# Kernel optimization log

Measured on AMD Instinct MI355X. Metric: run time of the kernel, lower is better.

Reference implementation:

```python
import jax, jax.numpy as jnp
import numpy as np


def setup_inputs() -> dict:
    key = jax.random.key(0)
    k1, k2, k3, k4, k5 = jax.random.split(key, 5)
    N, L, H = 512, 512, 768
    num_texts = 32
    hidden_states = jax.random.normal(k1, (N, L, H), dtype=jnp.float32)
    attention_mask = jax.random.randint(k2, (N, L), 0, 2).astype(jnp.int32)
    sample_map = jnp.sort(jax.random.randint(k3, (N,), 0, num_texts).astype(jnp.int64))
    Wq = jax.random.normal(k4, (H, H), dtype=jnp.float32) * (1.0 / np.sqrt(H))
    bq = jnp.zeros((H,), dtype=jnp.float32)
    Wk = jax.random.normal(k5, (H, H), dtype=jnp.float32) * (1.0 / np.sqrt(H))
    bk = jnp.zeros((H,), dtype=jnp.float32)
    return {
        'hidden_states': hidden_states,
        'attention_mask': attention_mask,
        'sample_map': sample_map,
        'Wq': Wq, 'bq': bq, 'Wk': Wk, 'bk': bk,
        'num_texts': num_texts,
    }


def _attn_pool(hidden_states, mask, Wq, bq, Wk, bk):
    # hidden_states: [N, L, H]; mask: [N, L]
    H = hidden_states.shape[-1]
    # Q from mean over sequence (unmasked mean, as in original)
    q = jnp.einsum('nh,oh->no', hidden_states.mean(axis=1), Wq) + bq   # [N, H]
    k = jnp.einsum('nlh,oh->nlo', hidden_states, Wk) + bk              # [N, L, H]
    scores = jnp.einsum('nh,nlh->nl', q, k) / jnp.sqrt(jnp.float32(H))  # [N, L]
    scores = jnp.where(mask == 0, jnp.float32(-1e9), scores)
    alphas = jax.nn.softmax(scores, axis=1)                            # [N, L]
    return jnp.einsum('nl,nlh->nh', alphas, hidden_states)             # [N, H]


def reference(hidden_states, attention_mask, sample_map, Wq, bq, Wk, bk, num_texts):
    # dropout is identity in eval mode
    pooled = _attn_pool(hidden_states, attention_mask, Wq, bq, Wk, bk)  # [N, H]
    seg = sample_map.astype(jnp.int32)
    sums = jax.ops.segment_sum(pooled, seg, num_segments=num_texts)     # [T, H]
    counts = jax.ops.segment_sum(jnp.ones((pooled.shape[0],), pooled.dtype), seg,
                                 num_segments=num_texts)                # [T]
    counts = jnp.clip(counts, 1.0, None)
    return sums / counts[:, None]
```

## Files before the change

### kernel.cpp

```cpp
#include <hip/hip_runtime.h>
#include <math.h>

#define HDIM 768
#define NG   192
#define LMAX 512

__device__ __forceinline__ float dot4(const float4 a, const float4 b) {
  return a.x * b.x + a.y * b.y + a.z * b.z + a.w * b.w;
}
__device__ __forceinline__ void fma4(float4& a, const float s, const float4 b) {
  a.x += s * b.x; a.y += s * b.y; a.z += s * b.z; a.w += s * b.w;
}
__device__ __forceinline__ void scale4(float4& a, const float s) {
  a.x *= s; a.y *= s; a.z *= s; a.w *= s;
}

__global__ __launch_bounds__(256) void detect_slots(const unsigned* __restrict__ mask_w,
                                                    const unsigned* __restrict__ smap_w,
                                                    unsigned* __restrict__ slots,
                                                    int mask_words, int smap_words) {
  __shared__ unsigned red[2];
  const int b = blockIdx.x, tid = threadIdx.x;
  if (tid < 2) red[tid] = 0;
  __syncthreads();
  const int gtid = b * 256 + tid, gsz = gridDim.x * 256;
  unsigned acc = 0;
  for (int i = gtid; i < mask_words / 2; i += gsz) acc |= mask_w[2 * i + 1];
  unsigned acc2 = 0;
  for (int i = gtid; i < smap_words / 2; i += gsz) acc2 |= smap_w[2 * i + 1];
  if (acc)  atomicOr(&red[0], 1u);
  if (acc2) atomicOr(&red[1], 1u);
  __syncthreads();
  if (tid == 0) { slots[b] = red[0]; slots[64 + b] = red[1]; }
}

__global__ __launch_bounds__(256) void prep_wc(const float* __restrict__ Wq,
                                               const float* __restrict__ Wk,
                                               const float* __restrict__ bq,
                                               float* __restrict__ Wc,
                                               float* __restrict__ c0, int H) {
  __shared__ float As[16][33];
  __shared__ float Bs[16][65];
  __shared__ float bqs[16];
  const int i0 = blockIdx.x * 32, j0 = blockIdx.y * 64;
  const int idx = threadIdx.x;
  const int li = idx & 31, lk = idx >> 5;
  const int lj = idx & 63, lk2 = idx >> 6;
  const int tc = idx & 15, tr = idx >> 4;
  float c[2][4] = {{0.f,0.f,0.f,0.f},{0.f,0.f,0.f,0.f}};
  float cb[4] = {0.f,0.f,0.f,0.f};
  const bool bias_lane = (blockIdx.x == 0) && (tr == 0);
  for (int o0 = 0; o0 < H; o0 += 16) {
    __syncthreads();
    As[lk][li]       = Wq[(size_t)(o0 + lk) * H + i0 + li];
    As[lk + 8][li]   = Wq[(size_t)(o0 + lk + 8) * H + i0 + li];
    Bs[lk2][lj]      = Wk[(size_t)(o0 + lk2) * H + j0 + lj];
    Bs[lk2 + 4][lj]  = Wk[(size_t)(o0 + lk2 + 4) * H + j0 + lj];
    Bs[lk2 + 8][lj]  = Wk[(size_t)(o0 + lk2 + 8) * H + j0 + lj];
    Bs[lk2 + 12][lj] = Wk[(size_t)(o0 + lk2 + 12) * H + j0 + lj];
    if (idx < 16) bqs[idx] = bq[o0 + idx];
    __syncthreads();
#pragma unroll
    for (int k = 0; k < 16; ++k) {
      const float a0 = As[k][tr * 2], a1 = As[k][tr * 2 + 1];
      const float b0 = Bs[k][tc * 4],     b1 = Bs[k][tc * 4 + 1];
      const float b2 = Bs[k][tc * 4 + 2], b3 = Bs[k][tc * 4 + 3];
      c[0][0] += a0 * b0; c[0][1] += a0 * b1; c[0][2] += a0 * b2; c[0][3] += a0 * b3;
      c[1][0] += a1 * b0; c[1][1] += a1 * b1; c[1][2] += a1 * b2; c[1][3] += a1 * b3;
      if (bias_lane) {
        const float bv = bqs[k];
        cb[0] += bv * b0; cb[1] += bv * b1; cb[2] += bv * b2; cb[3] += bv * b3;
      }
    }
  }
#pragma unroll
  for (int j = 0; j < 4; ++j) {
    Wc[(size_t)(i0 + tr * 2) * H + j0 + tc * 4 + j]     = c[0][j];
    Wc[(size_t)(i0 + tr * 2 + 1) * H + j0 + tc * 4 + j] = c[1][j];
  }
  if (bias_lane) {
#pragma unroll
    for (int j = 0; j < 4; ++j) c0[j0 + tc * 4 + j] = cb[j];
  }
}

__global__ __launch_bounds__(384) void fused(const float* __restrict__ hs,
                                             const unsigned* __restrict__ mask_w,
                                             const float* __restrict__ Wc,
                                             const float* __restrict__ c0,
                                             const unsigned* __restrict__ slots,
                                             float* __restrict__ pooled, int L) {
  __shared__ float4 red2[NG];
  __shared__ float4 meanv4[NG];
  __shared__ float4 vv4[NG];
  __shared__ float4 redv4[6][NG];
  __shared__ float mw[6], sw[6];
  __shared__ int   mrow[LMAX];
  __shared__ unsigned mfl;
  const int n = blockIdx.x, tid = threadIdx.x;
  const int w = tid >> 6, lane = tid & 63;

  if (tid == 0) mfl = 0u;
  __syncthreads();
  if (tid < 64 && slots[tid]) atomicOr(&mfl, 1u);

  const int half = tid / NG, t = tid - half * NG;
  const float4* hb = reinterpret_cast<const float4*>(hs) + (size_t)n * L * NG;
  float ax = 0.f, ay = 0.f, az = 0.f, aw = 0.f;
  int l = half;
  for (; l + 16 <= L; l += 16) {
    float4 u[8];
#pragma unroll
    for (int i = 0; i < 8; ++i) u[i] = hb[(size_t)(l + 2 * i) * NG + t];
#pragma unroll
    for (int i = 0; i < 8; ++i) { ax += u[i].x; ay += u[i].y; az += u[i].z; aw += u[i].w; }
  }
  for (; l < L; l += 2) {
    float4 u = hb[(size_t)l * NG + t];
    ax += u.x; ay += u.y; az += u.z; aw += u.w;
  }
  if (half == 1) { float4 o; o.x = ax; o.y = ay; o.z = az; o.w = aw; red2[t] = o; }
  __syncthreads();

  if (half == 0) {
    const float inv = 1.0f / (float)L;
    const float4 r = red2[t];
    float4 o;
    o.x = (ax + r.x) * inv; o.y = (ay + r.y) * inv;
    o.z = (az + r.z) * inv; o.w = (aw + r.w) * inv;
    meanv4[t] = o;
  }
  const int mask_is_i32 = (mfl != 0);
  for (int tt = tid; tt < L; tt += 384) {
    const size_t idx = (size_t)n * L + tt;
    mrow[tt] = (int)(mask_is_i32 ? mask_w[idx] : mask_w[2 * idx]);
  }
  __syncthreads();

  {
    const int c1 = tid, c2 = tid + 384;
    float acc1 = 0.f, acc2 = 0.f;
    const float* wp = Wc;
    for (int o = 0; o < HDIM; o += 4) {
      const float4 mv = meanv4[o >> 2];
      acc1 += mv.x * wp[c1] + mv.y * wp[HDIM + c1] + mv.z * wp[2 * HDIM + c1] + mv.w * wp[3 * HDIM + c1];
      acc2 += mv.x * wp[c2] + mv.y * wp[HDIM + c2] + mv.z * wp[2 * HDIM + c2] + mv.w * wp[3 * HDIM + c2];
      wp += 4 * HDIM;
    }
    ((float*)vv4)[c1] = acc1 + c0[c1];
    ((float*)vv4)[c2] = acc2 + c0[c2];
  }
  __syncthreads();

  const float4 vf0 = vv4[lane], vf1 = vv4[64 + lane], vf2 = vv4[128 + lane];
  const float scale = 1.0f / sqrtf((float)HDIM);
  const int cnt = (L - 1 - w) / 6 + 1;
  float m = -3.0e38f, ss = 0.f;
  float4 A0 = {0,0,0,0}, A1 = {0,0,0,0}, A2 = {0,0,0,0};
  float4 xa[2][3], xb[2][3];

  auto ld = [&](float4 (&X)[2][3], int j) {
#pragma unroll
    for (int u = 0; u < 2; ++u) {
      const int jj = j + u;
      const int rr = (jj < cnt) ? (L - 1 - 6 * jj - w) : 0;
      const float4* rp = hb + (size_t)rr * NG;
      X[u][0] = rp[lane]; X[u][1] = rp[64 + lane]; X[u][2] = rp[128 + lane];
    }
  };
  auto pr = [&](float4 (&X)[2][3], int j) {
    float s[2]; bool val[2];
#pragma unroll
    for (int u = 0; u < 2; ++u) {
      const int jj = j + u;
      val[u] = (jj < cnt);
      const int r = L - 1 - 6 * jj - w;
      float p = dot4(X[u][0], vf0) + dot4(X[u][1], vf1) + dot4(X[u][2], vf2);
#pragma unroll
      for (int off = 32; off > 0; off >>= 1) p += __shfl_xor(p, off, 64);
      s[u] = (!val[u] || mrow[r & (LMAX - 1)] == 0) ? -1e9f : p * scale;
    }
    const float mc = fmaxf(s[0], s[1]);
    if (mc > m) {
      const float f = __expf(m - mc);
      ss *= f; scale4(A0, f); scale4(A1, f); scale4(A2, f);
      m = mc;
    }
#pragma unroll
    for (int u = 0; u < 2; ++u) {
      const float pq = val[u] ? __expf(s[u] - m) : 0.f;
      ss += pq;
      fma4(A0, pq, X[u][0]); fma4(A1, pq, X[u][1]); fma4(A2, pq, X[u][2]);
    }
  };

  ld(xa, 0);
  for (int j = 0; j < 88; j += 4) {
    ld(xb, j + 2);
    pr(xa, j);
    if (j + 4 < 88) ld(xa, j + 4);
    pr(xb, j + 2);
  }

  if (lane == 0) { mw[w] = m; sw[w] = ss; }
  redv4[w][lane]       = A0;
  redv4[w][64 + lane]  = A1;
  redv4[w][128 + lane] = A2;
  __syncthreads();
  float M = mw[0];
#pragma unroll
  for (int j = 1; j < 6; ++j) M = fmaxf(M, mw[j]);
  float f[6], S = 0.f;
#pragma unroll
  for (int j = 0; j < 6; ++j) { f[j] = __expf(mw[j] - M); S += sw[j] * f[j]; }
  const float invS = 1.0f / S;
  const float* redp = (const float*)redv4;
#pragma unroll
  for (int part = 0; part < 2; ++part) {
    const int col = part * 384 + tid;
    float o = 0.f;
#pragma unroll
    for (int j = 0; j < 6; ++j) o += redp[j * HDIM + col] * f[j];
    pooled[(size_t)n * HDIM + col] = o * invS;
  }
}

__global__ __launch_bounds__(256) void segmean(const float* __restrict__ pooled,
                                               const void* __restrict__ smap,
                                               const unsigned* __restrict__ slots_s,
                                               float* __restrict__ out, int N) {
  __shared__ unsigned fsh;
  const int t = blockIdx.x, tid = threadIdx.x;
  const int col = blockIdx.y * 256 + tid;
  if (tid == 0) {
    unsigned f = 0;
    for (int i = 0; i < 64; ++i) f |= slots_s[i];
    fsh = f;
  }
  __syncthreads();
  const int smap_is_i32 = (fsh != 0);
  float a = 0.f;
  int cnt = 0;
  for (int i = 0; i < N; ++i) {
    const int s = smap_is_i32 ? ((const int*)smap)[i]
                              : (int)((const long long*)smap)[i];
    if (s == t) { a += pooled[(size_t)i * HDIM + col]; ++cnt; }
  }
  out[(size_t)t * HDIM + col] = a / (float)(cnt > 0 ? cnt : 1);
}

extern "C" void kernel_launch(void* const* d_in, const int* in_sizes, int n_in,
                              void* d_out, int out_size, void* d_ws, size_t ws_size,
                              hipStream_t stream) {
  const float*    hs     = (const float*)d_in[0];
  const unsigned* mask_w = (const unsigned*)d_in[1];
  const void*     smap   = d_in[2];
  const float*    Wq     = (const float*)d_in[3];
  const float*    bq     = (const float*)d_in[4];
  const float*    Wk     = (const float*)d_in[5];

  const int N = in_sizes[2];
  const int L = in_sizes[1] / N;
  const int H = in_sizes[4];
  const int T = out_size / H;

  float* Wc     = (float*)d_ws;
  float* c0     = Wc + (size_t)H * H;
  float* pooled = c0 + H;
  unsigned* slots = (unsigned*)(pooled + (size_t)N * H);
  (void)ws_size; (void)n_in;

  detect_slots<<<64, 256, 0, stream>>>(mask_w, (const unsigned*)smap, slots, N * L, N);
  prep_wc<<<dim3(H / 32, H / 64), 256, 0, stream>>>(Wq, Wk, bq, Wc, c0, H);
  fused<<<N, 384, 0, stream>>>(hs, mask_w, Wc, c0, slots, pooled, L);
  segmean<<<dim3(T, 3), 256, 0, stream>>>(pooled, smap, slots + 64, (float*)d_out, N);
}
```

Baseline: 419.7 us.

## Split fused pooling into mean, batched GEMM, and half-sequence pool kernels

The per-sample fused kernel is split into four stages. A mean kernel sums each half of the sequence, a tiled GEMM computes the query-projected vectors for all samples at once instead of a per-block matvec, and a pool kernel runs two blocks per sample over sequence halves with online softmax. A merge step combines the two partial softmax states during the segment mean. This raises block count and replaces redundant per-block weight reads with one batched GEMM, but hidden_states is now streamed twice across separate kernels and there are extra launches and workspace traffic.

```diff
diff --git a/kernel.cpp b/kernel.cpp
--- a/kernel.cpp
+++ b/kernel.cpp
@@ -84,101 +84,130 @@
   }
 }
 
-__global__ __launch_bounds__(384) void fused(const float* __restrict__ hs,
-                                             const unsigned* __restrict__ mask_w,
+__global__ __launch_bounds__(384) void mean2(const float* __restrict__ hs,
+                                             float* __restrict__ part, int L) {
+  __shared__ float4 red2[NG];
+  const int n = blockIdx.x >> 1, half = blockIdx.x & 1;
+  const int tid = threadIdx.x;
+  const int sub = tid / NG, t = tid - sub * NG;
+  const int Lh = L / 2, r0 = half * Lh;
+  const float4* hb = reinterpret_cast<const float4*>(hs) + ((size_t)n * L + r0) * NG;
+  float ax = 0.f, ay = 0.f, az = 0.f, aw = 0.f;
+  int l = sub;
+  for (; l + 16 <= Lh; l += 16) {
+    float4 u[8];
+#pragma unroll
+    for (int i = 0; i < 8; ++i) u[i] = hb[(size_t)(l + 2 * i) * NG + t];
+#pragma unroll
+    for (int i = 0; i < 8; ++i) { ax += u[i].x; ay += u[i].y; az += u[i].z; aw += u[i].w; }
+  }
+  for (; l < Lh; l += 2) {
+    float4 u = hb[(size_t)l * NG + t];
+    ax += u.x; ay += u.y; az += u.z; aw += u.w;
+  }
+  if (sub == 1) { float4 o; o.x = ax; o.y = ay; o.z = az; o.w = aw; red2[t] = o; }
+  __syncthreads();
+  if (sub == 0) {
+    const float4 r = red2[t];
+    float4 o; o.x = ax + r.x; o.y = ay + r.y; o.z = az + r.z; o.w = aw + r.w;
+    reinterpret_cast<float4*>(part + (size_t)(n * 2 + half) * HDIM)[t] = o;
+  }
+}
+
+__global__ __launch_bounds__(256) void gemmV(const float* __restrict__ P,
                                              const float* __restrict__ Wc,
                                              const float* __restrict__ c0,
-                                             const unsigned* __restrict__ slots,
-                                             float* __restrict__ pooled, int L) {
-  __shared__ float4 red2[NG];
-  __shared__ float4 meanv4[NG];
-  __shared__ float4 vv4[NG];
-  __shared__ float4 redv4[6][NG];
-  __shared__ float mw[6], sw[6];
-  __shared__ int   mrow[LMAX];
+                                             float* __restrict__ V,
+                                             int M, int Nn, int K, float invL) {
+  __shared__ float As[32][17];
+  __shared__ float Bs[16][65];
+  const int m0 = blockIdx.x * 32, n0 = blockIdx.y * 64;
+  const int idx = threadIdx.x;
+  const int lc = idx & 15, lr = idx >> 4;
+  const int bc = idx & 63, br = idx >> 6;
+  const int tc = idx & 15, tr = idx >> 4;
+  float c[2][4] = {{0.f,0.f,0.f,0.f},{0.f,0.f,0.f,0.f}};
+  for (int k0 = 0; k0 < K; k0 += 16) {
+    __syncthreads();
+    {
+      const int m1 = m0 + lr, m2 = m0 + lr + 16;
+      As[lr][lc]      = (P[(size_t)(2 * m1) * K + k0 + lc] + P[(size_t)(2 * m1 + 1) * K + k0 + lc]) * invL;
+      As[lr + 16][lc] = (P[(size_t)(2 * m2) * K + k0 + lc] + P[(size_t)(2 * m2 + 1) * K + k0 + lc]) * invL;
+    }
+    Bs[br][bc]      = Wc[(size_t)(k0 + br) * Nn + n0 + bc];
+    Bs[br + 4][bc]  = Wc[(size_t)(k0 + br + 4) * Nn + n0 + bc];
+    Bs[br + 8][bc]  = Wc[(size_t)(k0 + br + 8) * Nn + n0 + bc];
+    Bs[br + 12][bc] = Wc[(size_t)(k0 + br + 12) * Nn + n0 + bc];
+    __syncthreads();
+#pragma unroll
+    for (int k = 0; k < 16; ++k) {
+      const float a0 = As[tr * 2][k], a1 = As[tr * 2 + 1][k];
+      const float b0 = Bs[k][tc * 4], b1 = Bs[k][tc * 4 + 1];
+      const float b2 = Bs[k][tc * 4 + 2], b3 = Bs[k][tc * 4 + 3];
+      c[0][0] += a0 * b0; c[0][1] += a0 * b1; c[0][2] += a0 * b2; c[0][3] += a0 * b3;
+      c[1][0] += a1 * b0; c[1][1] += a1 * b1; c[1][2] += a1 * b2; c[1][3] += a1 * b3;
+    }
+  }
+#pragma unroll
+  for (int j = 0; j < 4; ++j) {
+    const float bv = c0[n0 + tc * 4 + j];
+    V[(size_t)(m0 + tr * 2) * Nn + n0 + tc * 4 + j]     = c[0][j] + bv;
+    V[(size_t)(m0 + tr * 2 + 1) * Nn + n0 + tc * 4 + j] = c[1][j] + bv;
+  }
+}
+
+__global__ __launch_bounds__(256) void pool(const float* __restrict__ hs,
+                                            const unsigned* __restrict__ mask_w,
+                                            const float* __restrict__ V,
+                                            const unsigned* __restrict__ slots,
+                                            float* __restrict__ acc_out,
+                                            float* __restrict__ ms_out, int L) {
+  __shared__ int   mrow[256];
+  __shared__ float4 redv[4][NG];
+  __shared__ float mw[4], sw[4];
   __shared__ unsigned mfl;
-  const int n = blockIdx.x, tid = threadIdx.x;
-  const int w = tid >> 6, lane = tid & 63;
+  const int bid = blockIdx.x;
+  const int n = bid >> 1, half = bid & 1;
+  const int tid = threadIdx.x, w = tid >> 6, lane = tid & 63;
+  const int Lh = L / 2, r0 = half * Lh;
 
   if (tid == 0) mfl = 0u;
   __syncthreads();
   if (tid < 64 && slots[tid]) atomicOr(&mfl, 1u);
-
-  const int half = tid / NG, t = tid - half * NG;
-  const float4* hb = reinterpret_cast<const float4*>(hs) + (size_t)n * L * NG;
-  float ax = 0.f, ay = 0.f, az = 0.f, aw = 0.f;
-  int l = half;
-  for (; l + 16 <= L; l += 16) {
-    float4 u[8];
-#pragma unroll
-    for (int i = 0; i < 8; ++i) u[i] = hb[(size_t)(l + 2 * i) * NG + t];
-#pragma unroll
-    for (int i = 0; i < 8; ++i) { ax += u[i].x; ay += u[i].y; az += u[i].z; aw += u[i].w; }
-  }
-  for (; l < L; l += 2) {
-    float4 u = hb[(size_t)l * NG + t];
-    ax += u.x; ay += u.y; az += u.z; aw += u.w;
-  }
-  if (half == 1) { float4 o; o.x = ax; o.y = ay; o.z = az; o.w = aw; red2[t] = o; }
-  __syncthreads();
-
-  if (half == 0) {
-    const float inv = 1.0f / (float)L;
-    const float4 r = red2[t];
-    float4 o;
-    o.x = (ax + r.x) * inv; o.y = (ay + r.y) * inv;
-    o.z = (az + r.z) * inv; o.w = (aw + r.w) * inv;
-    meanv4[t] = o;
-  }
+  __syncthreads();
   const int mask_is_i32 = (mfl != 0);
-  for (int tt = tid; tt < L; tt += 384) {
-    const size_t idx = (size_t)n * L + tt;
-    mrow[tt] = (int)(mask_is_i32 ? mask_w[idx] : mask_w[2 * idx]);
-  }
-  __syncthreads();
-
   {
-    const int c1 = tid, c2 = tid + 384;
-    float acc1 = 0.f, acc2 = 0.f;
-    const float* wp = Wc;
-    for (int o = 0; o < HDIM; o += 4) {
-      const float4 mv = meanv4[o >> 2];
-      acc1 += mv.x * wp[c1] + mv.y * wp[HDIM + c1] + mv.z * wp[2 * HDIM + c1] + mv.w * wp[3 * HDIM + c1];
-      acc2 += mv.x * wp[c2] + mv.y * wp[HDIM + c2] + mv.z * wp[2 * HDIM + c2] + mv.w * wp[3 * HDIM + c2];
-      wp += 4 * HDIM;
-    }
-    ((float*)vv4)[c1] = acc1 + c0[c1];
-    ((float*)vv4)[c2] = acc2 + c0[c2];
-  }
-  __syncthreads();
-
-  const float4 vf0 = vv4[lane], vf1 = vv4[64 + lane], vf2 = vv4[128 + lane];
+    const size_t idx = (size_t)n * L + r0 + tid;
+    mrow[tid] = (int)(mask_is_i32 ? mask_w[idx] : mask_w[2 * idx]);
+  }
+  __syncthreads();
+
+  const float4* v4 = reinterpret_cast<const float4*>(V + (size_t)n * HDIM);
+  const float4 vf0 = v4[lane], vf1 = v4[64 + lane], vf2 = v4[128 + lane];
+  const float4* hb = reinterpret_cast<const float4*>(hs) + ((size_t)n * L + r0) * NG;
   const float scale = 1.0f / sqrtf((float)HDIM);
-  const int cnt = (L - 1 - w) / 6 + 1;
+
   float m = -3.0e38f, ss = 0.f;
   float4 A0 = {0,0,0,0}, A1 = {0,0,0,0}, A2 = {0,0,0,0};
   float4 xa[2][3], xb[2][3];
 
-  auto ld = [&](float4 (&X)[2][3], int j) {
+  auto ld = [&](float4 (&X)[2][3], int b) {
 #pragma unroll
     for (int u = 0; u < 2; ++u) {
-      const int jj = j + u;
-      const int rr = (jj < cnt) ? (L - 1 - 6 * jj - w) : 0;
+      const int rr = Lh - 1 - 4 * (2 * b + u) - w;
       const float4* rp = hb + (size_t)rr * NG;
       X[u][0] = rp[lane]; X[u][1] = rp[64 + lane]; X[u][2] = rp[128 + lane];
     }
   };
-  auto pr = [&](float4 (&X)[2][3], int j) {
-    float s[2]; bool val[2];
+  auto pr = [&](float4 (&X)[2][3], int b) {
+    float s[2];
 #pragma unroll
     for (int u = 0; u < 2; ++u) {
-      const int jj = j + u;
-      val[u] = (jj < cnt);
-      const int r = L - 1 - 6 * jj - w;
+      const int rr = Lh - 1 - 4 * (2 * b + u) - w;
       float p = dot4(X[u][0], vf0) + dot4(X[u][1], vf1) + dot4(X[u][2], vf2);
 #pragma unroll
       for (int off = 32; off > 0; off >>= 1) p += __shfl_xor(p, off, 64);
-      s[u] = (!val[u] || mrow[r & (LMAX - 1)] == 0) ? -1e9f : p * scale;
+      s[u] = (mrow[rr] == 0) ? -1e9f : p * scale;
     }
     const float mc = fmaxf(s[0], s[1]);
     if (mc > m) {
@@ -188,47 +217,46 @@
     }
 #pragma unroll
     for (int u = 0; u < 2; ++u) {
-      const float pq = val[u] ? __expf(s[u] - m) : 0.f;
+      const float pq = __expf(s[u] - m);
       ss += pq;
       fma4(A0, pq, X[u][0]); fma4(A1, pq, X[u][1]); fma4(A2, pq, X[u][2]);
     }
   };
 
   ld(xa, 0);
-  for (int j = 0; j < 88; j += 4) {
-    ld(xb, j + 2);
-    pr(xa, j);
-    if (j + 4 < 88) ld(xa, j + 4);
-    pr(xb, j + 2);
+  const int nb = Lh / 8;
+  for (int b = 0; b < nb; b += 2) {
+    ld(xb, b + 1);
+    pr(xa, b);
+    if (b + 2 < nb) ld(xa, b + 2);
+    pr(xb, b + 1);
   }
 
   if (lane == 0) { mw[w] = m; sw[w] = ss; }
-  redv4[w][lane]       = A0;
-  redv4[w][64 + lane]  = A1;
-  redv4[w][128 + lane] = A2;
-  __syncthreads();
-  float M = mw[0];
-#pragma unroll
-  for (int j = 1; j < 6; ++j) M = fmaxf(M, mw[j]);
-  float f[6], S = 0.f;
-#pragma unroll
-  for (int j = 0; j < 6; ++j) { f[j] = __expf(mw[j] - M); S += sw[j] * f[j]; }
-  const float invS = 1.0f / S;
-  const float* redp = (const float*)redv4;
-#pragma unroll
-  for (int part = 0; part < 2; ++part) {
-    const int col = part * 384 + tid;
-    float o = 0.f;
-#pragma unroll
-    for (int j = 0; j < 6; ++j) o += redp[j * HDIM + col] * f[j];
-    pooled[(size_t)n * HDIM + col] = o * invS;
-  }
-}
-
-__global__ __launch_bounds__(256) void segmean(const float* __restrict__ pooled,
-                                               const void* __restrict__ smap,
-                                               const unsigned* __restrict__ slots_s,
-                                               float* __restrict__ out, int N) {
+  redv[w][lane]       = A0;
+  redv[w][64 + lane]  = A1;
+  redv[w][128 + lane] = A2;
+  __syncthreads();
+  const float M = fmaxf(fmaxf(mw[0], mw[1]), fmaxf(mw[2], mw[3]));
+  const float f0 = __expf(mw[0] - M), f1 = __expf(mw[1] - M);
+  const float f2 = __expf(mw[2] - M), f3 = __expf(mw[3] - M);
+  const float S = sw[0] * f0 + sw[1] * f1 + sw[2] * f2 + sw[3] * f3;
+  const float* redp = (const float*)redv;
+  const int pidx = n * 2 + half;
+#pragma unroll
+  for (int part = 0; part < 3; ++part) {
+    const int col = part * 256 + tid;
+    acc_out[(size_t)pidx * HDIM + col] =
+        redp[col] * f0 + redp[HDIM + col] * f1 + redp[2 * HDIM + col] * f2 + redp[3 * HDIM + col] * f3;
+  }
+  if (tid == 0) { ms_out[pidx * 2] = M; ms_out[pidx * 2 + 1] = S; }
+}
+
+__global__ __launch_bounds__(256) void merge_segmean(const float* __restrict__ acc,
+                                                     const float* __restrict__ ms,
+                                                     const void* __restrict__ smap,
+                                                     const unsigned* __restrict__ slots_s,
+                                                     float* __restrict__ out, int N) {
   __shared__ unsigned fsh;
   const int t = blockIdx.x, tid = threadIdx.x;
   const int col = blockIdx.y * 256 + tid;
@@ -244,7 +272,15 @@
   for (int i = 0; i < N; ++i) {
     const int s = smap_is_i32 ? ((const int*)smap)[i]
                               : (int)((const long long*)smap)[i];
-    if (s == t) { a += pooled[(size_t)i * HDIM + col]; ++cnt; }
+    if (s != t) continue;
+    const float m0 = ms[(i * 2) * 2],     q0 = ms[(i * 2) * 2 + 1];
+    const float m1 = ms[(i * 2 + 1) * 2], q1 = ms[(i * 2 + 1) * 2 + 1];
+    const float M = fmaxf(m0, m1);
+    const float f0 = __expf(m0 - M), f1 = __expf(m1 - M);
+    const float S = q0 * f0 + q1 * f1;
+    const float o = (acc[(size_t)(i * 2) * HDIM + col] * f0 +
+                     acc[(size_t)(i * 2 + 1) * HDIM + col] * f1) / S;
+    a += o; ++cnt;
   }
   out[(size_t)t * HDIM + col] = a / (float)(cnt > 0 ? cnt : 1);
 }
@@ -263,15 +299,21 @@
   const int L = in_sizes[1] / N;
   const int H = in_sizes[4];
   const int T = out_size / H;
-
-  float* Wc     = (float*)d_ws;
-  float* c0     = Wc + (size_t)H * H;
-  float* pooled = c0 + H;
-  unsigned* slots = (unsigned*)(pooled + (size_t)N * H);
+  const size_t NH = (size_t)N * H;
+
+  float* Wc   = (float*)d_ws;
+  float* c0   = Wc + (size_t)H * H;
+  float* part = c0 + H;
+  float* V    = part + 2 * NH;
+  float* acc  = V + NH;
+  float* ms   = acc + 2 * NH;
+  unsigned* slots = (unsigned*)(ms + 4 * N);
   (void)ws_size; (void)n_in;
 
   detect_slots<<<64, 256, 0, stream>>>(mask_w, (const unsigned*)smap, slots, N * L, N);
   prep_wc<<<dim3(H / 32, H / 64), 256, 0, stream>>>(Wq, Wk, bq, Wc, c0, H);
-  fused<<<N, 384, 0, stream>>>(hs, mask_w, Wc, c0, slots, pooled, L);
-  segmean<<<dim3(T, 3), 256, 0, stream>>>(pooled, smap, slots + 64, (float*)d_out, N);
-}
+  mean2<<<2 * N, 384, 0, stream>>>(hs, part, L);
+  gemmV<<<dim3(N / 32, H / 64), 256, 0, stream>>>(part, Wc, c0, V, N, H, H, 1.0f / (float)L);
+  pool<<<2 * N, 256, 0, stream>>>(hs, mask_w, V, slots, acc, ms, L);
+  merge_segmean<<<dim3(T, 3), 256, 0, stream>>>(acc, ms, smap, slots + 64, (float*)d_out, N);
+}
```

Result: slower. 464.4 us (+10.7%).

## Prefetch first rows before the vector GEMV, vectorize GEMV, deepen mean-load unroll

Applied to the files above, without the earlier changes.

The first two batches of hidden-state rows are now loaded before the Wc·mean matrix-vector product, so their memory latency overlaps that compute. The GEMV itself is rewritten so each thread reads float4 weight rows and the two halves of the block are combined through shared memory. The load loop is also reordered to keep one batch prefetched ahead, and the mean-reduction unroll is doubled to keep more loads in flight. The cost is higher register pressure from the extra prefetched rows and wider unroll, which could reduce occupancy.

```diff
diff --git a/kernel.cpp b/kernel.cpp
--- a/kernel.cpp
+++ b/kernel.cpp
@@ -108,12 +108,12 @@
   const float4* hb = reinterpret_cast<const float4*>(hs) + (size_t)n * L * NG;
   float ax = 0.f, ay = 0.f, az = 0.f, aw = 0.f;
   int l = half;
-  for (; l + 16 <= L; l += 16) {
-    float4 u[8];
-#pragma unroll
-    for (int i = 0; i < 8; ++i) u[i] = hb[(size_t)(l + 2 * i) * NG + t];
-#pragma unroll
-    for (int i = 0; i < 8; ++i) { ax += u[i].x; ay += u[i].y; az += u[i].z; aw += u[i].w; }
+  for (; l + 32 <= L; l += 32) {
+    float4 u[16];
+#pragma unroll
+    for (int i = 0; i < 16; ++i) u[i] = hb[(size_t)(l + 2 * i) * NG + t];
+#pragma unroll
+    for (int i = 0; i < 16; ++i) { ax += u[i].x; ay += u[i].y; az += u[i].z; aw += u[i].w; }
   }
   for (; l < L; l += 2) {
     float4 u = hb[(size_t)l * NG + t];
@@ -137,27 +137,12 @@
   }
   __syncthreads();
 
-  {
-    const int c1 = tid, c2 = tid + 384;
-    float acc1 = 0.f, acc2 = 0.f;
-    const float* wp = Wc;
-    for (int o = 0; o < HDIM; o += 4) {
-      const float4 mv = meanv4[o >> 2];
-      acc1 += mv.x * wp[c1] + mv.y * wp[HDIM + c1] + mv.z * wp[2 * HDIM + c1] + mv.w * wp[3 * HDIM + c1];
-      acc2 += mv.x * wp[c2] + mv.y * wp[HDIM + c2] + mv.z * wp[2 * HDIM + c2] + mv.w * wp[3 * HDIM + c2];
-      wp += 4 * HDIM;
-    }
-    ((float*)vv4)[c1] = acc1 + c0[c1];
-    ((float*)vv4)[c2] = acc2 + c0[c2];
-  }
-  __syncthreads();
-
-  const float4 vf0 = vv4[lane], vf1 = vv4[64 + lane], vf2 = vv4[128 + lane];
   const float scale = 1.0f / sqrtf((float)HDIM);
   const int cnt = (L - 1 - w) / 6 + 1;
   float m = -3.0e38f, ss = 0.f;
   float4 A0 = {0,0,0,0}, A1 = {0,0,0,0}, A2 = {0,0,0,0};
   float4 xa[2][3], xb[2][3];
+  float4 vf0, vf1, vf2;
 
   auto ld = [&](float4 (&X)[2][3], int j) {
 #pragma unroll
@@ -168,17 +153,44 @@
       X[u][0] = rp[lane]; X[u][1] = rp[64 + lane]; X[u][2] = rp[128 + lane];
     }
   };
+  ld(xa, 0);
+  ld(xb, 2);
+
+  {
+    const int par = tid / NG, g = tid - par * NG;
+    const float* mv = (const float*)meanv4;
+    const float4* Wc4 = reinterpret_cast<const float4*>(Wc);
+    float4 va = {0.f, 0.f, 0.f, 0.f};
+#pragma unroll 4
+    for (int o = par; o < HDIM; o += 2) {
+      const float mo = mv[o];
+      const float4 wr = Wc4[(size_t)o * NG + g];
+      va.x += mo * wr.x; va.y += mo * wr.y; va.z += mo * wr.z; va.w += mo * wr.w;
+    }
+    if (par == 1) red2[g] = va;
+    __syncthreads();
+    if (par == 0) {
+      const float4 r = red2[g];
+      const float4 cc = reinterpret_cast<const float4*>(c0)[g];
+      float4 o4;
+      o4.x = va.x + r.x + cc.x; o4.y = va.y + r.y + cc.y;
+      o4.z = va.z + r.z + cc.z; o4.w = va.w + r.w + cc.w;
+      vv4[g] = o4;
+    }
+    __syncthreads();
+  }
+  vf0 = vv4[lane]; vf1 = vv4[64 + lane]; vf2 = vv4[128 + lane];
+
   auto pr = [&](float4 (&X)[2][3], int j) {
-    float s[2]; bool val[2];
+    float s[2]; 
 #pragma unroll
     for (int u = 0; u < 2; ++u) {
       const int jj = j + u;
-      val[u] = (jj < cnt);
       const int r = L - 1 - 6 * jj - w;
       float p = dot4(X[u][0], vf0) + dot4(X[u][1], vf1) + dot4(X[u][2], vf2);
 #pragma unroll
       for (int off = 32; off > 0; off >>= 1) p += __shfl_xor(p, off, 64);
-      s[u] = (!val[u] || mrow[r & (LMAX - 1)] == 0) ? -1e9f : p * scale;
+      s[u] = (jj >= cnt || mrow[r & (LMAX - 1)] == 0) ? -1e9f : p * scale;
     }
     const float mc = fmaxf(s[0], s[1]);
     if (mc > m) {
@@ -188,18 +200,17 @@
     }
 #pragma unroll
     for (int u = 0; u < 2; ++u) {
-      const float pq = val[u] ? __expf(s[u] - m) : 0.f;
+      const float pq = (j + u < cnt) ? __expf(s[u] - m) : 0.f;
       ss += pq;
       fma4(A0, pq, X[u][0]); fma4(A1, pq, X[u][1]); fma4(A2, pq, X[u][2]);
     }
   };
 
-  ld(xa, 0);
   for (int j = 0; j < 88; j += 4) {
-    ld(xb, j + 2);
     pr(xa, j);
     if (j + 4 < 88) ld(xa, j + 4);
     pr(xb, j + 2);
+    if (j + 6 < 88) ld(xb, j + 6);
   }
 
   if (lane == 0) { mw[w] = m; sw[w] = ss; }
```

Result: slower. 433.5 us (+3.3%).
